# Kernel optimization log

Measured on AMD Instinct MI355X. Metric: run time of the kernel, lower is better.

The kernel has to match this reference:

```python
import jax, jax.numpy as jnp
import numpy as np
from jax import lax

B, N, DIM = 32, 3136, 320
HEADS = 5
C_RATIO = 1.25
C_NEW = int(DIM * C_RATIO)  # 400
SR = 4
SCALE = ((DIM // HEADS) * C_RATIO) ** -0.5  # (64*1.25)^-0.5 = 80^-0.5


def setup_inputs() -> dict:
    key = jax.random.key(0)
    ks = jax.random.split(key, 12)
    s = 0.05
    return {
        "x": jax.random.normal(ks[0], (B, N, DIM), dtype=jnp.float32),
        "H": 56,
        "W": 56,
        # depthwise conv: kernel 4x4, stride 4, groups=DIM -> OIHW with I=1
        "dw_w": jax.random.normal(ks[1], (DIM, 1, SR, SR), dtype=jnp.float32) * s,
        "dw_b": jnp.zeros((DIM,), dtype=jnp.float32),
        # pointwise 1x1 conv DIM -> C_NEW (stored as [out, in])
        "pw_w": jax.random.normal(ks[2], (C_NEW, DIM), dtype=jnp.float32) * s,
        "pw_b": jnp.zeros((C_NEW,), dtype=jnp.float32),
        "ln_g": jnp.ones((C_NEW,), dtype=jnp.float32),
        "ln_b": jnp.zeros((C_NEW,), dtype=jnp.float32),
        # linear weights stored [in, out], no bias (qkv_bias=False)
        "q_w": jax.random.normal(ks[3], (DIM, C_NEW), dtype=jnp.float32) * s,
        "k_w": jax.random.normal(ks[4], (C_NEW, C_NEW), dtype=jnp.float32) * s,
        "v_w": jax.random.normal(ks[5], (C_NEW, DIM), dtype=jnp.float32) * s,
        "proj_w": jax.random.normal(ks[6], (DIM, DIM), dtype=jnp.float32) * s,
        "proj_b": jnp.zeros((DIM,), dtype=jnp.float32),
    }


def _layernorm(x, g, b, eps=1e-5):
    mu = jnp.mean(x, axis=-1, keepdims=True)
    var = jnp.mean(jnp.square(x - mu), axis=-1, keepdims=True)
    return (x - mu) * lax.rsqrt(var + eps) * g + b


def reference(x, H, W, dw_w, dw_b, pw_w, pw_b, ln_g, ln_b, q_w, k_w, v_w, proj_w, proj_b):
    Bz, Nn, C = x.shape
    dq = C_NEW // HEADS  # 80 (q/k head dim)
    dv = C // HEADS      # 64 (v head dim)

    # q: [B, heads, N, dq]
    q = jnp.einsum("bnc,cd->bnd", x, q_w).reshape(Bz, Nn, HEADS, dq).transpose(0, 2, 1, 3)

    # spatial reduction: dwconv (k=SR, s=SR, groups=C) then 1x1 conv to C_NEW
    xs = x.transpose(0, 2, 1).reshape(Bz, C, H, W)
    xs = lax.conv_general_dilated(
        xs, dw_w, window_strides=(SR, SR), padding="VALID",
        feature_group_count=C, dimension_numbers=("NCHW", "OIHW", "NCHW"),
    ) + dw_b[None, :, None, None]
    xs = jnp.einsum("bchw,dc->bdhw", xs, pw_w) + pw_b[None, :, None, None]
    Nk = xs.shape[2] * xs.shape[3]
    xs = xs.reshape(Bz, C_NEW, Nk).transpose(0, 2, 1)  # [B, Nk, C_NEW]

    xs = jax.nn.gelu(_layernorm(xs, ln_g, ln_b), approximate=False)

    k = jnp.einsum("bkc,cd->bkd", xs, k_w).reshape(Bz, Nk, HEADS, dq).transpose(0, 2, 1, 3)
    v = jnp.einsum("bkc,cd->bkd", xs, v_w).reshape(Bz, Nk, HEADS, dv).transpose(0, 2, 1, 3)

    attn = jax.nn.softmax(jnp.einsum("bhqd,bhkd->bhqk", q, k) * SCALE, axis=-1)
    out = jnp.einsum("bhqk,bhkd->bhqd", attn, v)  # [B, heads, N, dv]
    out = out.transpose(0, 2, 1, 3).reshape(Bz, Nn, C)
    return jnp.einsum("bnc,cd->bnd", out, proj_w) + proj_b
```

## Files before the change

kernel.cpp:

```cpp
#include <hip/hip_runtime.h>
#include <math.h>

#define NB 32
#define NN 3136
#define CD 320
#define NH 5
#define CN 400
#define NKEY 196
#define DQ 80
#define DV 64
#define SCALE_F 0.11180339887498949f

typedef __bf16 bf16x8 __attribute__((ext_vector_type(8)));
typedef float f32x4 __attribute__((ext_vector_type(4)));
typedef unsigned short u16;
typedef unsigned int u32;

__device__ __forceinline__ u16 f2bf(float f) {
  u32 u = __float_as_uint(f);
  u += 0x7fffu + ((u >> 16) & 1u);
  return (u16)(u >> 16);
}

__device__ __forceinline__ uint2 pack4(float a, float b, float c, float d) {
  return make_uint2((u32)f2bf(a) | ((u32)f2bf(b) << 16),
                    (u32)f2bf(c) | ((u32)f2bf(d) << 16));
}

__global__ void k_prep(const float* __restrict__ q_w,
                       const float* __restrict__ proj_w,
                       const float* __restrict__ k_w,
                       const float* __restrict__ v_w,
                       const float* __restrict__ pw_w, u16* __restrict__ qwT,
                       u16* __restrict__ pwT, u16* __restrict__ kvwT,
                       u16* __restrict__ pwb) {
  const int i0 = blockIdx.x * 256 + threadIdx.x;
  const int stride = gridDim.x * 256;
  for (int idx = i0; idx < 400 * 320; idx += stride) {
    const int o = idx / 320, c = idx - o * 320;
    qwT[idx] = f2bf(q_w[(size_t)c * 400 + o]);
  }
  for (int idx = i0; idx < 320 * 320; idx += stride) {
    const int o = idx / 320, c = idx - o * 320;
    pwT[idx] = f2bf(proj_w[(size_t)c * 320 + o]);
  }
  for (int idx = i0; idx < 400 * 320; idx += stride) {
    pwb[idx] = f2bf(pw_w[idx]);
  }
  for (int idx = i0; idx < 720 * 416; idx += stride) {
    const int o = idx / 416, c = idx - o * 416;
    float v = 0.f;
    if (c < 400) v = (o < 400) ? k_w[(size_t)c * 400 + o] : v_w[(size_t)c * 320 + (o - 400)];
    kvwT[idx] = f2bf(v);
  }
}

__global__ __launch_bounds__(256) void k_dw(const float* __restrict__ x,
                                            const float* __restrict__ dw_w,
                                            const float* __restrict__ dw_b,
                                            u16* __restrict__ dwc16,
                                            u16* __restrict__ xbf) {
  const int idx = blockIdx.x * 256 + threadIdx.x;
  const int row = idx / 80, c4 = (idx - row * 80) * 4;
  const int b = row / 196, pl = row - b * 196;
  const int oh = pl / 14, ow = pl - oh * 14;
  const size_t pix0 = (size_t)b * NN + (size_t)(oh * 4) * 56 + ow * 4;
  const float* xb = x + pix0 * CD + c4;

  float w[4][16];
#pragma unroll
  for (int k = 0; k < 4; k++)
#pragma unroll
    for (int j4 = 0; j4 < 4; j4++)
      *(float4*)&w[k][j4 * 4] = *(const float4*)(dw_w + (c4 + k) * 16 + j4 * 4);

  float a0 = dw_b[c4], a1 = dw_b[c4 + 1], a2 = dw_b[c4 + 2], a3 = dw_b[c4 + 3];
#pragma unroll
  for (int i = 0; i < 4; i++)
#pragma unroll
    for (int j = 0; j < 4; j++) {
      const float4 xv = *(const float4*)(xb + (size_t)(i * 56 + j) * CD);
      const int t = i * 4 + j;
      a0 += xv.x * w[0][t];
      a1 += xv.y * w[1][t];
      a2 += xv.z * w[2][t];
      a3 += xv.w * w[3][t];
      *(uint2*)(xbf + (pix0 + i * 56 + j) * CN + c4) =
          pack4(xv.x, xv.y, xv.z, xv.w);
    }
  *(uint2*)(dwc16 + (size_t)row * 416 + c4) = pack4(a0, a1, a2, a3);
}

__global__ __launch_bounds__(64) void k_pwln(u16* xs,
                                             const u16* __restrict__ pwb,
                                             const float* __restrict__ pw_b,
                                             const float* __restrict__ ln_g,
                                             const float* __restrict__ ln_b) {
  const int lane = threadIdx.x & 63;
  const int quad = lane >> 4, l15 = lane & 15;
  const int row0 = blockIdx.x * 16;
  const f32x4 fz = {0.f, 0.f, 0.f, 0.f};

  bf16x8 Bfr[10];
  {
    const u16* xr = xs + (size_t)(row0 + l15) * 416;
#pragma unroll
    for (int ks = 0; ks < 10; ks++)
      Bfr[ks] = *(const bf16x8*)(xr + ks * 32 + quad * 8);
  }
  f32x4 acc[25];
#pragma unroll
  for (int n = 0; n < 25; n++) acc[n] = fz;
#pragma unroll 1
  for (int n = 0; n < 25; n++) {
    const u16* wr = pwb + (size_t)(n * 16 + l15) * CD;
#pragma unroll
    for (int ks = 0; ks < 10; ks++) {
      const bf16x8 A = *(const bf16x8*)(wr + ks * 32 + quad * 8);
      acc[n] = __builtin_amdgcn_mfma_f32_16x16x32_bf16(A, Bfr[ks], acc[n], 0, 0, 0);
    }
    const float4 pb = *(const float4*)(pw_b + n * 16 + quad * 4);
    acc[n][0] += pb.x; acc[n][1] += pb.y; acc[n][2] += pb.z; acc[n][3] += pb.w;
  }
  float s = 0.f, ss = 0.f;
#pragma unroll
  for (int n = 0; n < 25; n++)
#pragma unroll
    for (int r = 0; r < 4; r++) {
      s += acc[n][r];
      ss += acc[n][r] * acc[n][r];
    }
  s += __shfl_xor(s, 16); ss += __shfl_xor(ss, 16);
  s += __shfl_xor(s, 32); ss += __shfl_xor(ss, 32);
  const float mu = s * (1.f / 400.f);
  const float var = ss * (1.f / 400.f) - mu * mu;
  const float rstd = rsqrtf(var + 1e-5f);

  u16* orow = xs + (size_t)(row0 + l15) * 416;
#pragma unroll 1
  for (int n = 0; n < 25; n++) {
    const float4 g = *(const float4*)(ln_g + n * 16 + quad * 4);
    const float4 bb = *(const float4*)(ln_b + n * 16 + quad * 4);
    float ge[4];
#pragma unroll
    for (int r = 0; r < 4; r++) {
      const float gg = (&g.x)[r], bv = (&bb.x)[r];
      const float v = (acc[n][r] - mu) * rstd * gg + bv;
      ge[r] = 0.5f * v * (1.f + erff(v * 0.70710678118654752f));
    }
    *(uint2*)(orow + n * 16 + quad * 4) = pack4(ge[0], ge[1], ge[2], ge[3]);
  }
  *(uint2*)(orow + 400 + quad * 4) = make_uint2(0, 0);
}

__global__ __launch_bounds__(64) void k_kv(const u16* __restrict__ xs,
                                           const u16* __restrict__ kvwT,
                                           u16* __restrict__ kb,
                                           u16* __restrict__ vt) {
  const int lane = threadIdx.x & 63;
  const int quad = lane >> 4, l15 = lane & 15;
  const int mt = blockIdx.x;
  const f32x4 fz = {0.f, 0.f, 0.f, 0.f};

  bf16x8 A[13];
  {
    const u16* xr = xs + (size_t)(mt * 16 + l15) * 416;
#pragma unroll
    for (int ks = 0; ks < 13; ks++)
      A[ks] = *(const bf16x8*)(xr + ks * 32 + quad * 8);
  }
#pragma unroll 1
  for (int n = 0; n < 15; n++) {
    const int nt = blockIdx.y * 15 + n;
    f32x4 acc = fz;
    const u16* wr = kvwT + (size_t)(nt * 16 + l15) * 416;
#pragma unroll
    for (int ks = 0; ks < 13; ks++) {
      const bf16x8 B = *(const bf16x8*)(wr + ks * 32 + quad * 8);
      acc = __builtin_amdgcn_mfma_f32_16x16x32_bf16(A[ks], B, acc, 0, 0, 0);
    }
    const int col = nt * 16 + l15;
    if (col < 400) {
#pragma unroll
      for (int r = 0; r < 4; r++)
        kb[(size_t)(mt * 16 + quad * 4 + r) * 400 + col] = f2bf(acc[r]);
    } else {
      const int vo = col - 400;
#pragma unroll
      for (int r = 0; r < 4; r++) {
        const int row = mt * 16 + quad * 4 + r;
        const int bb = row / 196, key = row - bb * 196;
        vt[((size_t)(bb * 320 + vo)) * 224 + key] = f2bf(acc[r]);
      }
    }
  }
}

__global__ __launch_bounds__(256) void k_q(u16* qb,
                                           const u16* __restrict__ qwT) {
  __shared__ u16 wlds[2][5120];
  const int tid = threadIdx.x, lane = tid & 63;
  const int wv = tid >> 6, quad = lane >> 4, l15 = lane & 15;
  const int r0 = blockIdx.x * 128 + wv * 32;
  const f32x4 fz = {0.f, 0.f, 0.f, 0.f};

  bf16x8 Bfr[2][10];
#pragma unroll
  for (int t = 0; t < 2; t++) {
    const u16* xr = qb + (size_t)(r0 + t * 16 + l15) * CN;
#pragma unroll
    for (int ks = 0; ks < 10; ks++)
      Bfr[t][ks] = *(const bf16x8*)(xr + ks * 32 + quad * 8);
  }

  for (int idx = tid; idx < 640; idx += 256)
    *(uint4*)(wlds[0] + idx * 8) = *(const uint4*)(
        qwT + (size_t)(idx & 15) * CD + (idx >> 6) * 32 + ((idx >> 4) & 3) * 8);
  __syncthreads();

#pragma unroll 1
  for (int n = 0; n < 25; n++) {
    const u16* wb = wlds[n & 1];
    uint4 st0, st1, st2;
    const bool h2 = tid < 128;
    if (n < 24) {
      const int base = (n + 1) * 16;
      {
        const int idx = tid;
        st0 = *(const uint4*)(qwT + (size_t)(base + (idx & 15)) * CD +
                              (idx >> 6) * 32 + ((idx >> 4) & 3) * 8);
      }
      {
        const int idx = tid + 256;
        st1 = *(const uint4*)(qwT + (size_t)(base + (idx & 15)) * CD +
                              (idx >> 6) * 32 + ((idx >> 4) & 3) * 8);
      }
      if (h2) {
        const int idx = tid + 512;
        st2 = *(const uint4*)(qwT + (size_t)(base + (idx & 15)) * CD +
                              (idx >> 6) * 32 + ((idx >> 4) & 3) * 8);
      }
    }
    f32x4 acc[2] = {fz, fz};
#pragma unroll
    for (int ks = 0; ks < 10; ks++) {
      const bf16x8 A = *(const bf16x8*)(wb + ks * 512 + lane * 8);
      acc[0] = __builtin_amdgcn_mfma_f32_16x16x32_bf16(A, Bfr[0][ks], acc[0], 0, 0, 0);
      acc[1] = __builtin_amdgcn_mfma_f32_16x16x32_bf16(A, Bfr[1][ks], acc[1], 0, 0, 0);
    }
#pragma unroll
    for (int t = 0; t < 2; t++)
      *(uint2*)(qb + (size_t)(r0 + t * 16 + l15) * CN + n * 16 + quad * 4) =
          pack4(acc[t][0], acc[t][1], acc[t][2], acc[t][3]);
    if (n < 24) {
      u16* wn = wlds[(n + 1) & 1];
      *(uint4*)(wn + tid * 8) = st0;
      *(uint4*)(wn + (tid + 256) * 8) = st1;
      if (h2) *(uint4*)(wn + (tid + 512) * 8) = st2;
      __syncthreads();
    }
  }
}

__global__ __launch_bounds__(256, 5) void k_attn(u16* __restrict__ qb,
                                                 const u16* __restrict__ kb,
                                                 const u16* __restrict__ vt) {
  const int h = blockIdx.x, qt = blockIdx.y, b = blockIdx.z;
  const int tid = threadIdx.x, lane = tid & 63, wv = tid >> 6;
  const int quad = lane >> 4, l15 = lane & 15;
  const int q0 = qt * 64, m0 = wv * 16;
  const f32x4 fz = {0.f, 0.f, 0.f, 0.f};

  __shared__ u16 Ks[196 * 80];

  for (int idx = tid; idx < 1960; idx += 256) {
    const int key = idx / 10, g = idx - key * 10;
    *(uint4*)(Ks + idx * 8) =
        *(const uint4*)(kb + ((size_t)(b * NKEY + key)) * CN + h * DQ + g * 8);
  }
  __syncthreads();

  f32x4 sacc[13];
#pragma unroll
  for (int n = 0; n < 13; n++) sacc[n] = fz;
  {
    union { uint4 u; bf16x8 v; } z;
    z.u = make_uint4(0, 0, 0, 0);
    const u16* qr = qb + (size_t)(b * NN + q0 + m0 + l15) * CN + h * DQ;
    bf16x8 bq0 = *(const bf16x8*)(qr + quad * 8);
    bf16x8 bq1 = *(const bf16x8*)(qr + 32 + quad * 8);
    bf16x8 bq2 = (quad < 2) ? *(const bf16x8*)(qr + 64 + quad * 8) : z.v;
#pragma unroll
    for (int n = 0; n < 13; n++) {
      const int rr = n * 16 + l15;
      const u16* kr = Ks + ((rr > 195) ? 195 : rr) * 80;
      sacc[n] = __builtin_amdgcn_mfma_f32_16x16x32_bf16(
          *(const bf16x8*)(kr + quad * 8), bq0, sacc[n], 0, 0, 0);
      sacc[n] = __builtin_amdgcn_mfma_f32_16x16x32_bf16(
          *(const bf16x8*)(kr + 32 + quad * 8), bq1, sacc[n], 0, 0, 0);
      const bf16x8 ak2 = (quad < 2) ? *(const bf16x8*)(kr + 64 + quad * 8) : z.v;
      sacc[n] = __builtin_amdgcn_mfma_f32_16x16x32_bf16(ak2, bq2, sacc[n], 0, 0, 0);
    }
  }

  u32 u[13][2];
  {
    float mx = -1e30f;
#pragma unroll
    for (int n = 0; n < 13; n++)
#pragma unroll
      for (int r = 0; r < 4; r++) {
        float s = sacc[n][r] * SCALE_F;
        if (n == 12 && quad != 0) s = -1e30f;
        sacc[n][r] = s;
        mx = fmaxf(mx, s);
      }
    mx = fmaxf(mx, __shfl_xor(mx, 16));
    mx = fmaxf(mx, __shfl_xor(mx, 32));
    float sum = 0.f;
#pragma unroll
    for (int n = 0; n < 13; n++)
#pragma unroll
      for (int r = 0; r < 4; r++) {
        const float e = __expf(sacc[n][r] - mx);
        sacc[n][r] = e;
        sum += e;
      }
    sum += __shfl_xor(sum, 16);
    sum += __shfl_xor(sum, 32);
    const float inv = 1.f / sum;
#pragma unroll
    for (int n = 0; n < 13; n++) {
      u[n][0] = (u32)f2bf(sacc[n][0] * inv) | ((u32)f2bf(sacc[n][1] * inv) << 16);
      u[n][1] = (u32)f2bf(sacc[n][2] * inv) | ((u32)f2bf(sacc[n][3] * inv) << 16);
    }
  }

  f32x4 oacc[4];
#pragma unroll
  for (int nn = 0; nn < 4; nn++) oacc[nn] = fz;
  {
    const u16* vbase = vt + (size_t)(b * 320 + h * DV) * 224;
    const int src0 = ((lane & 16) << 1) | l15;
    const int src1 = src0 + 16;
    const bool hi = (quad >= 2);
#pragma unroll
    for (int kk = 0; kk < 7; kk++) {
      union { bf16x8 v; u32 w[4]; } bp;
      const u32 a0 = (u32)__shfl((int)u[2 * kk][0], src0);
      const u32 a1 = (u32)__shfl((int)u[2 * kk][1], src0);
      const u32 a2 = (u32)__shfl((int)u[2 * kk][0], src1);
      const u32 a3 = (u32)__shfl((int)u[2 * kk][1], src1);
      u32 b0 = 0, b1 = 0, b2 = 0, b3 = 0;
      if (kk < 6) {
        b0 = (u32)__shfl((int)u[2 * kk + 1][0], src0);
        b1 = (u32)__shfl((int)u[2 * kk + 1][1], src0);
        b2 = (u32)__shfl((int)u[2 * kk + 1][0], src1);
        b3 = (u32)__shfl((int)u[2 * kk + 1][1], src1);
      }
      bp.w[0] = hi ? b0 : a0;
      bp.w[1] = hi ? b1 : a1;
      bp.w[2] = hi ? b2 : a2;
      bp.w[3] = hi ? b3 : a3;
#pragma unroll
      for (int nn = 0; nn < 4; nn++) {
        const bf16x8 A = *(const bf16x8*)(vbase + (size_t)(nn * 16 + l15) * 224 +
                                          kk * 32 + quad * 8);
        oacc[nn] = __builtin_amdgcn_mfma_f32_16x16x32_bf16(A, bp.v, oacc[nn], 0, 0, 0);
      }
    }
  }
  u16* orow = qb + (size_t)(b * NN + q0 + m0 + l15) * CN + h * DQ;
#pragma unroll
  for (int nn = 0; nn < 4; nn++)
    *(uint2*)(orow + nn * 16 + quad * 4) =
        pack4(oacc[nn][0], oacc[nn][1], oacc[nn][2], oacc[nn][3]);
}

__global__ __launch_bounds__(256) void k_proj(const u16* __restrict__ ao,
                                              const u16* __restrict__ pwT,
                                              const float* __restrict__ proj_b,
                                              float* __restrict__ out) {
  __shared__ u16 wlds[2][5120];
  const int tid = threadIdx.x, lane = tid & 63;
  const int wv = tid >> 6, quad = lane >> 4, l15 = lane & 15;
  const int r0 = blockIdx.x * 128 + wv * 32;
  const f32x4 fz = {0.f, 0.f, 0.f, 0.f};

  bf16x8 Bfr[2][10];
#pragma unroll
  for (int t = 0; t < 2; t++) {
    const u16* xr = ao + (size_t)(r0 + t * 16 + l15) * CN;
#pragma unroll
    for (int ks = 0; ks < 10; ks++)
      Bfr[t][ks] = *(const bf16x8*)(xr + (ks >> 1) * DQ + (ks & 1) * 32 + quad * 8);
  }

  for (int idx = tid; idx < 640; idx += 256)
    *(uint4*)(wlds[0] + idx * 8) = *(const uint4*)(
        pwT + (size_t)(idx & 15) * CD + (idx >> 6) * 32 + ((idx >> 4) & 3) * 8);
  __syncthreads();

#pragma unroll 1
  for (int n = 0; n < 20; n++) {
    const u16* wb = wlds[n & 1];
    uint4 st0, st1, st2;
    const bool h2 = tid < 128;
    if (n < 19) {
      const int base = (n + 1) * 16;
      {
        const int idx = tid;
        st0 = *(const uint4*)(pwT + (size_t)(base + (idx & 15)) * CD +
                              (idx >> 6) * 32 + ((idx >> 4) & 3) * 8);
      }
      {
        const int idx = tid + 256;
        st1 = *(const uint4*)(pwT + (size_t)(base + (idx & 15)) * CD +
                              (idx >> 6) * 32 + ((idx >> 4) & 3) * 8);
      }
      if (h2) {
        const int idx = tid + 512;
        st2 = *(const uint4*)(pwT + (size_t)(base + (idx & 15)) * CD +
                              (idx >> 6) * 32 + ((idx >> 4) & 3) * 8);
      }
    }
    f32x4 acc[2] = {fz, fz};
#pragma unroll
    for (int ks = 0; ks < 10; ks++) {
      const bf16x8 A = *(const bf16x8*)(wb + ks * 512 + lane * 8);
      acc[0] = __builtin_amdgcn_mfma_f32_16x16x32_bf16(A, Bfr[0][ks], acc[0], 0, 0, 0);
      acc[1] = __builtin_amdgcn_mfma_f32_16x16x32_bf16(A, Bfr[1][ks], acc[1], 0, 0, 0);
    }
    const float4 pb = *(const float4*)(proj_b + n * 16 + quad * 4);
#pragma unroll
    for (int t = 0; t < 2; t++) {
      float4 o;
      o.x = acc[t][0] + pb.x;
      o.y = acc[t][1] + pb.y;
      o.z = acc[t][2] + pb.z;
      o.w = acc[t][3] + pb.w;
      *(float4*)(out + (size_t)(r0 + t * 16 + l15) * CD + n * 16 + quad * 4) = o;
    }
    if (n < 19) {
      u16* wn = wlds[(n + 1) & 1];
      *(uint4*)(wn + tid * 8) = st0;
      *(uint4*)(wn + (tid + 256) * 8) = st1;
      if (h2) *(uint4*)(wn + (tid + 512) * 8) = st2;
      __syncthreads();
    }
  }
}

extern "C" void kernel_launch(void* const* d_in, const int* in_sizes, int n_in,
                              void* d_out, int out_size, void* d_ws,
                              size_t ws_size, hipStream_t stream) {
  const float* x = (const float*)d_in[0];
  const float* dw_w = (const float*)d_in[3];
  const float* dw_b = (const float*)d_in[4];
  const float* pw_w = (const float*)d_in[5];
  const float* pw_b = (const float*)d_in[6];
  const float* ln_g = (const float*)d_in[7];
  const float* ln_b = (const float*)d_in[8];
  const float* q_w = (const float*)d_in[9];
  const float* k_w = (const float*)d_in[10];
  const float* v_w = (const float*)d_in[11];
  const float* proj_w = (const float*)d_in[12];
  const float* proj_b = (const float*)d_in[13];
  float* out = (float*)d_out;

  u16* w = (u16*)d_ws;
  u16* xs16 = w;
  u16* kb16 = xs16 + 2609152;
  u16* vt16 = kb16 + 2508800;
  u16* qb16 = vt16 + 2293760;
  u16* qwT = qb16 + 40140864;
  u16* pwT = qwT + 128000;
  u16* kvwT = pwT + 102400;
  u16* pwb = kvwT + 299520;

  k_prep<<<512, 256, 0, stream>>>(q_w, proj_w, k_w, v_w, pw_w, qwT, pwT, kvwT,
                                  pwb);
  k_dw<<<1960, 256, 0, stream>>>(x, dw_w, dw_b, xs16 ,
                                 qb16 );
  k_pwln<<<392, 64, 0, stream>>>(xs16, pwb, pw_b, ln_g, ln_b);
  k_kv<<<dim3(392, 3), 64, 0, stream>>>(xs16, kvwT, kb16, vt16);
  k_q<<<784, 256, 0, stream>>>(qb16, qwT);
  k_attn<<<dim3(NH, 49, NB), 256, 0, stream>>>(qb16, kb16, vt16);
  k_proj<<<784, 256, 0, stream>>>(qb16, pwT, proj_b, out);
}
```

Baseline: 584.9 us.

## Spread pointwise-LN and KV projection kernels across four waves per block

k_pwln now runs 256 threads per block. Each of the four waves computes a strided subset of the 25 output tiles, and the LayerNorm row statistics are combined through a small shared-memory reduction before GELU. k_kv now groups four M-tiles per block. The kvwT weight tiles are staged once into double-buffered LDS, prefetched into registers while the MFMAs run, and shared by all four waves instead of being re-read from global memory by each single-wave block. The aim is more parallelism and less weight traffic in these small pre-attention kernels, at the cost of block barriers and LDS use.

```diff
diff --git a/kernel.cpp b/kernel.cpp
--- a/kernel.cpp
+++ b/kernel.cpp
@@ -91,12 +91,13 @@
   *(uint2*)(dwc16 + (size_t)row * 416 + c4) = pack4(a0, a1, a2, a3);
 }
 
-__global__ __launch_bounds__(64) void k_pwln(u16* xs,
-                                             const u16* __restrict__ pwb,
-                                             const float* __restrict__ pw_b,
-                                             const float* __restrict__ ln_g,
-                                             const float* __restrict__ ln_b) {
-  const int lane = threadIdx.x & 63;
+__global__ __launch_bounds__(256) void k_pwln(u16* xs,
+                                              const u16* __restrict__ pwb,
+                                              const float* __restrict__ pw_b,
+                                              const float* __restrict__ ln_g,
+                                              const float* __restrict__ ln_b) {
+  __shared__ float redS[4][16], redQ[4][16];
+  const int tid = threadIdx.x, lane = tid & 63, wv = tid >> 6;
   const int quad = lane >> 4, l15 = lane & 15;
   const int row0 = blockIdx.x * 16;
   const f32x4 fz = {0.f, 0.f, 0.f, 0.f};
@@ -108,58 +109,73 @@
     for (int ks = 0; ks < 10; ks++)
       Bfr[ks] = *(const bf16x8*)(xr + ks * 32 + quad * 8);
   }
-  f32x4 acc[25];
-#pragma unroll
-  for (int n = 0; n < 25; n++) acc[n] = fz;
-#pragma unroll 1
-  for (int n = 0; n < 25; n++) {
-    const u16* wr = pwb + (size_t)(n * 16 + l15) * CD;
-#pragma unroll
-    for (int ks = 0; ks < 10; ks++) {
-      const bf16x8 A = *(const bf16x8*)(wr + ks * 32 + quad * 8);
-      acc[n] = __builtin_amdgcn_mfma_f32_16x16x32_bf16(A, Bfr[ks], acc[n], 0, 0, 0);
-    }
-    const float4 pb = *(const float4*)(pw_b + n * 16 + quad * 4);
-    acc[n][0] += pb.x; acc[n][1] += pb.y; acc[n][2] += pb.z; acc[n][3] += pb.w;
+  f32x4 acc[7];
+#pragma unroll
+  for (int j = 0; j < 7; j++) acc[j] = fz;
+#pragma unroll
+  for (int j = 0; j < 7; j++) {
+    const int n = wv + 4 * j;
+    if (n < 25) {
+      const u16* wr = pwb + (size_t)(n * 16 + l15) * CD;
+#pragma unroll
+      for (int ks = 0; ks < 10; ks++) {
+        const bf16x8 A = *(const bf16x8*)(wr + ks * 32 + quad * 8);
+        acc[j] = __builtin_amdgcn_mfma_f32_16x16x32_bf16(A, Bfr[ks], acc[j], 0, 0, 0);
+      }
+      const float4 pb = *(const float4*)(pw_b + n * 16 + quad * 4);
+      acc[j][0] += pb.x; acc[j][1] += pb.y; acc[j][2] += pb.z; acc[j][3] += pb.w;
+    }
   }
   float s = 0.f, ss = 0.f;
 #pragma unroll
-  for (int n = 0; n < 25; n++)
+  for (int j = 0; j < 7; j++)
 #pragma unroll
     for (int r = 0; r < 4; r++) {
-      s += acc[n][r];
-      ss += acc[n][r] * acc[n][r];
+      s += acc[j][r];
+      ss += acc[j][r] * acc[j][r];
     }
   s += __shfl_xor(s, 16); ss += __shfl_xor(ss, 16);
   s += __shfl_xor(s, 32); ss += __shfl_xor(ss, 32);
+  if (lane < 16) {
+    redS[wv][l15] = s;
+    redQ[wv][l15] = ss;
+  }
+  __syncthreads();
+  s = redS[0][l15] + redS[1][l15] + redS[2][l15] + redS[3][l15];
+  ss = redQ[0][l15] + redQ[1][l15] + redQ[2][l15] + redQ[3][l15];
   const float mu = s * (1.f / 400.f);
   const float var = ss * (1.f / 400.f) - mu * mu;
   const float rstd = rsqrtf(var + 1e-5f);
 
   u16* orow = xs + (size_t)(row0 + l15) * 416;
-#pragma unroll 1
-  for (int n = 0; n < 25; n++) {
-    const float4 g = *(const float4*)(ln_g + n * 16 + quad * 4);
-    const float4 bb = *(const float4*)(ln_b + n * 16 + quad * 4);
-    float ge[4];
-#pragma unroll
-    for (int r = 0; r < 4; r++) {
-      const float gg = (&g.x)[r], bv = (&bb.x)[r];
-      const float v = (acc[n][r] - mu) * rstd * gg + bv;
-      ge[r] = 0.5f * v * (1.f + erff(v * 0.70710678118654752f));
-    }
-    *(uint2*)(orow + n * 16 + quad * 4) = pack4(ge[0], ge[1], ge[2], ge[3]);
-  }
-  *(uint2*)(orow + 400 + quad * 4) = make_uint2(0, 0);
-}
-
-__global__ __launch_bounds__(64) void k_kv(const u16* __restrict__ xs,
-                                           const u16* __restrict__ kvwT,
-                                           u16* __restrict__ kb,
-                                           u16* __restrict__ vt) {
-  const int lane = threadIdx.x & 63;
+#pragma unroll
+  for (int j = 0; j < 7; j++) {
+    const int n = wv + 4 * j;
+    if (n < 25) {
+      const float4 g = *(const float4*)(ln_g + n * 16 + quad * 4);
+      const float4 bb = *(const float4*)(ln_b + n * 16 + quad * 4);
+      float ge[4];
+#pragma unroll
+      for (int r = 0; r < 4; r++) {
+        const float gg = (&g.x)[r], bv = (&bb.x)[r];
+        const float v = (acc[j][r] - mu) * rstd * gg + bv;
+        ge[r] = 0.5f * v * (1.f + erff(v * 0.70710678118654752f));
+      }
+      *(uint2*)(orow + n * 16 + quad * 4) = pack4(ge[0], ge[1], ge[2], ge[3]);
+    }
+  }
+  if (wv == 3) *(uint2*)(orow + 400 + quad * 4) = make_uint2(0, 0);
+}
+
+__global__ __launch_bounds__(256) void k_kv(const u16* __restrict__ xs,
+                                            const u16* __restrict__ kvwT,
+                                            u16* __restrict__ kb,
+                                            u16* __restrict__ vt) {
+  __shared__ u16 wlds[2][6656];
+  const int tid = threadIdx.x, lane = tid & 63, wv = tid >> 6;
   const int quad = lane >> 4, l15 = lane & 15;
-  const int mt = blockIdx.x;
+  const int mt = blockIdx.x * 4 + wv;
+  const int nt0 = blockIdx.y * 5;
   const f32x4 fz = {0.f, 0.f, 0.f, 0.f};
 
   bf16x8 A[13];
@@ -169,14 +185,47 @@
     for (int ks = 0; ks < 13; ks++)
       A[ks] = *(const bf16x8*)(xr + ks * 32 + quad * 8);
   }
+
+  for (int idx = tid; idx < 832; idx += 256) {
+    const int ks = idx >> 6, ln = idx & 63, q = ln >> 4, l = ln & 15;
+    *(uint4*)(wlds[0] + idx * 8) = *(const uint4*)(
+        kvwT + (size_t)(nt0 * 16 + l) * 416 + ks * 32 + q * 8);
+  }
+  __syncthreads();
+
 #pragma unroll 1
-  for (int n = 0; n < 15; n++) {
-    const int nt = blockIdx.y * 15 + n;
+  for (int j = 0; j < 5; j++) {
+    const int nt = nt0 + j;
+    const u16* wb = wlds[j & 1];
+    uint4 st0, st1, st2, st3;
+    const bool t4 = tid < 64;
+    if (j < 4) {
+      const int base = (nt + 1) * 16;
+      {
+        const int idx = tid;
+        const int ks = idx >> 6, ln = idx & 63, q = ln >> 4, l = ln & 15;
+        st0 = *(const uint4*)(kvwT + (size_t)(base + l) * 416 + ks * 32 + q * 8);
+      }
+      {
+        const int idx = tid + 256;
+        const int ks = idx >> 6, ln = idx & 63, q = ln >> 4, l = ln & 15;
+        st1 = *(const uint4*)(kvwT + (size_t)(base + l) * 416 + ks * 32 + q * 8);
+      }
+      {
+        const int idx = tid + 512;
+        const int ks = idx >> 6, ln = idx & 63, q = ln >> 4, l = ln & 15;
+        st2 = *(const uint4*)(kvwT + (size_t)(base + l) * 416 + ks * 32 + q * 8);
+      }
+      if (t4) {
+        const int idx = tid + 768;
+        const int ks = idx >> 6, ln = idx & 63, q = ln >> 4, l = ln & 15;
+        st3 = *(const uint4*)(kvwT + (size_t)(base + l) * 416 + ks * 32 + q * 8);
+      }
+    }
     f32x4 acc = fz;
-    const u16* wr = kvwT + (size_t)(nt * 16 + l15) * 416;
 #pragma unroll
     for (int ks = 0; ks < 13; ks++) {
-      const bf16x8 B = *(const bf16x8*)(wr + ks * 32 + quad * 8);
+      const bf16x8 B = *(const bf16x8*)(wb + ks * 512 + lane * 8);
       acc = __builtin_amdgcn_mfma_f32_16x16x32_bf16(A[ks], B, acc, 0, 0, 0);
     }
     const int col = nt * 16 + l15;
@@ -192,6 +241,14 @@
         const int bb = row / 196, key = row - bb * 196;
         vt[((size_t)(bb * 320 + vo)) * 224 + key] = f2bf(acc[r]);
       }
+    }
+    if (j < 4) {
+      u16* wn = wlds[(j + 1) & 1];
+      *(uint4*)(wn + tid * 8) = st0;
+      *(uint4*)(wn + (tid + 256) * 8) = st1;
+      *(uint4*)(wn + (tid + 512) * 8) = st2;
+      if (t4) *(uint4*)(wn + (tid + 768) * 8) = st3;
+      __syncthreads();
     }
   }
 }
@@ -482,8 +539,8 @@
                                   pwb);
   k_dw<<<1960, 256, 0, stream>>>(x, dw_w, dw_b, xs16 ,
                                  qb16 );
-  k_pwln<<<392, 64, 0, stream>>>(xs16, pwb, pw_b, ln_g, ln_b);
-  k_kv<<<dim3(392, 3), 64, 0, stream>>>(xs16, kvwT, kb16, vt16);
+  k_pwln<<<392, 256, 0, stream>>>(xs16, pwb, pw_b, ln_g, ln_b);
+  k_kv<<<dim3(98, 9), 256, 0, stream>>>(xs16, kvwT, kb16, vt16);
   k_q<<<784, 256, 0, stream>>>(qb16, qwT);
   k_attn<<<dim3(NH, 49, NB), 256, 0, stream>>>(qb16, kb16, vt16);
   k_proj<<<784, 256, 0, stream>>>(qb16, pwT, proj_b, out);
```

Result: faster. 538.4 us (-7.9%).
